# Performance work log

Measured on AMD Instinct MI355X. Metric: run time of the kernel, lower is better.

Reference implementation:

```python
import jax, jax.numpy as jnp
import numpy as np

N_NODES = 100000
N_EDGES = 1600000
IN_FEATS, HIDDEN, OUT_MU, OUT_LV = 256, 128, 64, 64


def setup_inputs() -> dict:
    key = jax.random.key(0)
    ks = jax.random.split(key, 8)
    X = jax.random.normal(ks[0], (N_NODES, IN_FEATS), dtype=jnp.float32)
    edge_index = jax.random.randint(ks[1], (2, N_EDGES), 0, N_NODES, dtype=jnp.int64)
    def glorot(k, shape):
        lim = np.sqrt(6.0 / (shape[0] + shape[1])).astype(np.float32)
        return jax.random.uniform(k, shape, jnp.float32, -lim, lim)
    W1 = glorot(ks[2], (IN_FEATS, HIDDEN))
    b1 = jnp.zeros((HIDDEN,), jnp.float32)
    Wmu = glorot(ks[3], (HIDDEN, OUT_MU))
    bmu = jnp.zeros((OUT_MU,), jnp.float32)
    Wlv = glorot(ks[4], (HIDDEN, OUT_LV))
    blv = jnp.zeros((OUT_LV,), jnp.float32)
    return {"X": X, "edge_index": edge_index, "W1": W1, "b1": b1,
            "Wmu": Wmu, "bmu": bmu, "Wlv": Wlv, "blv": blv}


def _gcn_norm(edge_index, num_nodes):
    # Add self-loops (PyG GCNConv default) and compute symmetric normalization.
    loop = jnp.arange(num_nodes, dtype=edge_index.dtype)
    row = jnp.concatenate([edge_index[0], loop])  # source
    col = jnp.concatenate([edge_index[1], loop])  # target
    deg = jax.ops.segment_sum(jnp.ones_like(col, dtype=jnp.float32), col,
                              num_segments=num_nodes)
    dinv = jnp.where(deg > 0, jax.lax.rsqrt(deg), 0.0)
    norm = dinv[row] * dinv[col]  # [E+N]
    return row, col, norm


def _gcn_conv(x, W, b, row, col, norm, num_nodes):
    # Linear transform, then normalized sparse neighbor aggregation at targets.
    h = x @ W                                   # [N, F_out]
    msg = h[row] * norm[:, None]                # gather + scale, [E+N, F_out]
    out = jax.ops.segment_sum(msg, col, num_segments=num_nodes)
    return out + b


def reference(X, edge_index, W1, b1, Wmu, bmu, Wlv, blv):
    n = X.shape[0]
    row, col, norm = _gcn_norm(edge_index, n)
    H = jax.nn.relu(_gcn_conv(X, W1, b1, row, col, norm, n))
    mu = _gcn_conv(H, Wmu, bmu, row, col, norm, n)
    lv = _gcn_conv(H, Wlv, blv, row, col, norm, n)
    return (mu, lv)
```

## Files before the change

kernel.cpp:

```cpp
#include <hip/hip_runtime.h>
#include <hip/hip_bf16.h>
#include <cstdint>

#define N_FEATS_IN 256
#define HID 128
#define OUTF 64
#define SITEMS 8

typedef __bf16 bf16x8 __attribute__((ext_vector_type(8)));
typedef __bf16 bf16x2 __attribute__((ext_vector_type(2)));
typedef float f32x4 __attribute__((ext_vector_type(4)));


__global__ __launch_bounds__(256) void count_deg_kernel(const int* __restrict__ ei, int E,
    int* __restrict__ deg, int* __restrict__ erank) {
  int e = blockIdx.x * 256 + threadIdx.x;
  if (e < E) erank[e] = atomicAdd(&deg[ei[E + e]], 1);
}

__global__ __launch_bounds__(256) void dinv_kernel(const int* __restrict__ deg,
                                                   float* __restrict__ dinv, int n) {
  int i = blockIdx.x * 256 + threadIdx.x;
  if (i < n) dinv[i] = rsqrtf((float)(deg[i] + 1));
}


__global__ __launch_bounds__(256) void scan_part_kernel(const int* __restrict__ cnt, int n,
                                                        int* __restrict__ bsum) {
  __shared__ int ts[256];
  const int t = threadIdx.x;
  int base = (blockIdx.x * 256 + t) * SITEMS;
  int s = 0;
#pragma unroll
  for (int i = 0; i < SITEMS; ++i) {
    int idx = base + i;
    if (idx < n) s += cnt[idx];
  }
  ts[t] = s;
  __syncthreads();
  for (int off = 128; off > 0; off >>= 1) {
    if (t < off) ts[t] += ts[t + off];
    __syncthreads();
  }
  if (t == 0) bsum[blockIdx.x] = ts[0];
}

__global__ __launch_bounds__(256) void scan_bsum_kernel(int* __restrict__ bsum, int nb) {
  __shared__ int ts[256];
  const int t = threadIdx.x;
  int v = (t < nb) ? bsum[t] : 0;
  ts[t] = v;
  __syncthreads();
  for (int off = 1; off < 256; off <<= 1) {
    int u = (t >= off) ? ts[t - off] : 0;
    __syncthreads();
    ts[t] += u;
    __syncthreads();
  }
  if (t < nb) bsum[t] = ts[t] - v;
}

__global__ __launch_bounds__(256) void scan_final_kernel(const int* __restrict__ cnt, int n,
    const int* __restrict__ bsum, int* __restrict__ ptr) {
  __shared__ int ts[256];
  const int t = threadIdx.x;
  int base = (blockIdx.x * 256 + t) * SITEMS;
  int loc[SITEMS];
  int s = 0;
#pragma unroll
  for (int i = 0; i < SITEMS; ++i) {
    int idx = base + i;
    loc[i] = (idx < n) ? cnt[idx] : 0;
    s += loc[i];
  }
  ts[t] = s;
  __syncthreads();
  for (int off = 1; off < 256; off <<= 1) {
    int u = (t >= off) ? ts[t - off] : 0;
    __syncthreads();
    ts[t] += u;
    __syncthreads();
  }
  int run = bsum[blockIdx.x] + ts[t] - s;
#pragma unroll
  for (int i = 0; i < SITEMS; ++i) {
    int idx = base + i;
    if (idx < n) ptr[idx] = run;
    run += loc[i];
  }
  if (base < n && base + SITEMS >= n) ptr[n] = run;
}


__global__ __launch_bounds__(256) void fill_kernel(const int* __restrict__ ei, int E,
    const int* __restrict__ ptr, const int* __restrict__ erank,
    const float* __restrict__ dinv, int2* __restrict__ erec) {
  int e = blockIdx.x * 256 + threadIdx.x;
  if (e < E) {
    int r = ei[e];
    int c = ei[E + e];
    int pos = ptr[c] + erank[e];
    int2 rec;
    rec.x = r;
    rec.y = __float_as_int(dinv[r] * dinv[c]);
    erec[pos] = rec;
  }
}


__global__ __launch_bounds__(256) void pack_w1_kernel(const float* __restrict__ W,
                                                      __bf16* __restrict__ Wp) {
  int idx = blockIdx.x * 256 + threadIdx.x;
  if (idx >= 32768) return;
  int j = idx & 7, l = (idx >> 3) & 63, t = (idx >> 9) & 7, s = idx >> 12;
  int k = s * 32 + (l >> 4) * 8 + j;
  int n = t * 16 + (l & 15);
  Wp[idx] = (__bf16)W[k * HID + n];
}

__global__ __launch_bounds__(256) void pack_wc_kernel(const float* __restrict__ Wmu,
    const float* __restrict__ Wlv, __bf16* __restrict__ Wp) {
  int idx = blockIdx.x * 256 + threadIdx.x;
  if (idx >= 16384) return;
  int j = idx & 7, l = (idx >> 3) & 63, t = (idx >> 9) & 7, s = idx >> 12;
  int k = s * 32 + (l >> 4) * 8 + j;
  int g = t * 16 + (l & 15);
  float v = (g < OUTF) ? Wmu[k * OUTF + g] : Wlv[k * OUTF + (g - OUTF)];
  Wp[idx] = (__bf16)v;
}


__global__ __launch_bounds__(256) void gemm1_mfma(const float* __restrict__ X,
    const __bf16* __restrict__ Wp, __bf16* __restrict__ Yb, int nrows) {
  const int lane = threadIdx.x & 63;
  const int wave = threadIdx.x >> 6;
  const int rb = blockIdx.x * 128 + wave * 32;
  const int lm = lane & 15;
  const int q = lane >> 4;

  f32x4 acc[2][8];
#pragma unroll
  for (int m = 0; m < 2; ++m)
#pragma unroll
    for (int t = 0; t < 8; ++t) acc[m][t] = (f32x4)0.f;

  int r0 = min(rb + lm, nrows - 1);
  int r1 = min(rb + 16 + lm, nrows - 1);
  const float* x0 = X + (size_t)r0 * N_FEATS_IN + q * 8;
  const float* x1 = X + (size_t)r1 * N_FEATS_IN + q * 8;
  const bf16x8* wp = (const bf16x8*)Wp;

#pragma unroll
  for (int s = 0; s < 8; ++s) {
    float4 u0 = ((const float4*)(x0 + s * 32))[0];
    float4 v0 = ((const float4*)(x0 + s * 32))[1];
    float4 u1 = ((const float4*)(x1 + s * 32))[0];
    float4 v1 = ((const float4*)(x1 + s * 32))[1];
    bf16x8 a0, a1;
    a0[0] = (__bf16)u0.x; a0[1] = (__bf16)u0.y; a0[2] = (__bf16)u0.z; a0[3] = (__bf16)u0.w;
    a0[4] = (__bf16)v0.x; a0[5] = (__bf16)v0.y; a0[6] = (__bf16)v0.z; a0[7] = (__bf16)v0.w;
    a1[0] = (__bf16)u1.x; a1[1] = (__bf16)u1.y; a1[2] = (__bf16)u1.z; a1[3] = (__bf16)u1.w;
    a1[4] = (__bf16)v1.x; a1[5] = (__bf16)v1.y; a1[6] = (__bf16)v1.z; a1[7] = (__bf16)v1.w;
#pragma unroll
    for (int t = 0; t < 8; ++t) {
      bf16x8 b = wp[(s * 8 + t) * 64 + lane];
      acc[0][t] = __builtin_amdgcn_mfma_f32_16x16x32_bf16(a0, b, acc[0][t], 0, 0, 0);
      acc[1][t] = __builtin_amdgcn_mfma_f32_16x16x32_bf16(a1, b, acc[1][t], 0, 0, 0);
    }
  }
#pragma unroll
  for (int m = 0; m < 2; ++m) {
    int rowbase = rb + m * 16 + q * 4;
#pragma unroll
    for (int t = 0; t < 8; ++t) {
#pragma unroll
      for (int r = 0; r < 4; ++r) {
        int row = rowbase + r;
        if (row < nrows) Yb[(size_t)row * HID + t * 16 + lm] = (__bf16)acc[m][t][r];
      }
    }
  }
}


__global__ __launch_bounds__(64) void agg_kernel(const __bf16* __restrict__ Fin,
    const int* __restrict__ ptr, const int2* __restrict__ erec,
    const float* __restrict__ dinv, const float* __restrict__ bias,
    __bf16* __restrict__ Fout, int do_relu) {
  const int c = blockIdx.x;
  const int t = threadIdx.x;
  const float d = dinv[c];
  bf16x2 sv = ((const bf16x2*)(Fin + (size_t)c * HID))[t];
  float ax = d * d * (float)sv[0];
  float ay = d * d * (float)sv[1];
  const int beg = ptr[c], end = ptr[c + 1];
  int e = beg;
  for (; e + 4 <= end; e += 4) {
    int2 p0 = erec[e], p1 = erec[e + 1], p2 = erec[e + 2], p3 = erec[e + 3];
    float n0 = __int_as_float(p0.y), n1 = __int_as_float(p1.y);
    float n2 = __int_as_float(p2.y), n3 = __int_as_float(p3.y);
    bf16x2 v0 = ((const bf16x2*)(Fin + (size_t)p0.x * HID))[t];
    bf16x2 v1 = ((const bf16x2*)(Fin + (size_t)p1.x * HID))[t];
    bf16x2 v2 = ((const bf16x2*)(Fin + (size_t)p2.x * HID))[t];
    bf16x2 v3 = ((const bf16x2*)(Fin + (size_t)p3.x * HID))[t];
    ax = fmaf(n0, (float)v0[0], ax); ay = fmaf(n0, (float)v0[1], ay);
    ax = fmaf(n1, (float)v1[0], ax); ay = fmaf(n1, (float)v1[1], ay);
    ax = fmaf(n2, (float)v2[0], ax); ay = fmaf(n2, (float)v2[1], ay);
    ax = fmaf(n3, (float)v3[0], ax); ay = fmaf(n3, (float)v3[1], ay);
  }
  for (; e < end; ++e) {
    int2 p = erec[e];
    float nn = __int_as_float(p.y);
    bf16x2 v = ((const bf16x2*)(Fin + (size_t)p.x * HID))[t];
    ax = fmaf(nn, (float)v[0], ax);
    ay = fmaf(nn, (float)v[1], ay);
  }
  if (do_relu) {
    ax = fmaxf(ax + bias[2 * t], 0.f);
    ay = fmaxf(ay + bias[2 * t + 1], 0.f);
  }
  bf16x2 o;
  o[0] = (__bf16)ax;
  o[1] = (__bf16)ay;
  ((bf16x2*)(Fout + (size_t)c * HID))[t] = o;
}


__global__ __launch_bounds__(256) void gemm2_mfma(const __bf16* __restrict__ Gb,
    const __bf16* __restrict__ Wp, const float* __restrict__ bmu,
    const float* __restrict__ blv, float* __restrict__ out, int nrows) {
  const int lane = threadIdx.x & 63;
  const int wave = threadIdx.x >> 6;
  const int rb = blockIdx.x * 128 + wave * 32;
  const int lm = lane & 15;
  const int q = lane >> 4;

  f32x4 acc[2][8];
#pragma unroll
  for (int m = 0; m < 2; ++m)
#pragma unroll
    for (int t = 0; t < 8; ++t) acc[m][t] = (f32x4)0.f;

  int r0 = min(rb + lm, nrows - 1);
  int r1 = min(rb + 16 + lm, nrows - 1);
  const __bf16* g0 = Gb + (size_t)r0 * HID + q * 8;
  const __bf16* g1 = Gb + (size_t)r1 * HID + q * 8;
  const bf16x8* wp = (const bf16x8*)Wp;

#pragma unroll
  for (int s = 0; s < 4; ++s) {
    bf16x8 a0 = *(const bf16x8*)(g0 + s * 32);
    bf16x8 a1 = *(const bf16x8*)(g1 + s * 32);
#pragma unroll
    for (int t = 0; t < 8; ++t) {
      bf16x8 b = wp[(s * 8 + t) * 64 + lane];
      acc[0][t] = __builtin_amdgcn_mfma_f32_16x16x32_bf16(a0, b, acc[0][t], 0, 0, 0);
      acc[1][t] = __builtin_amdgcn_mfma_f32_16x16x32_bf16(a1, b, acc[1][t], 0, 0, 0);
    }
  }
#pragma unroll
  for (int m = 0; m < 2; ++m) {
    int rowbase = rb + m * 16 + q * 4;
#pragma unroll
    for (int t = 0; t < 8; ++t) {
      int g = t * 16 + lm;
      float bv = (g < OUTF) ? bmu[g] : blv[g - OUTF];
      float* ob = (g < OUTF) ? (out + g) : (out + (size_t)nrows * OUTF + (g - OUTF));
#pragma unroll
      for (int r = 0; r < 4; ++r) {
        int row = rowbase + r;
        if (row < nrows) ob[(size_t)row * OUTF] = acc[m][t][r] + bv;
      }
    }
  }
}


extern "C" void kernel_launch(void* const* d_in, const int* in_sizes, int n_in,
                              void* d_out, int out_size, void* d_ws, size_t ws_size,
                              hipStream_t stream) {
  const float* X   = (const float*)d_in[0];
  const int*   ei  = (const int*)d_in[1];
  const float* W1  = (const float*)d_in[2];
  const float* b1  = (const float*)d_in[3];
  const float* Wmu = (const float*)d_in[4];
  const float* bmu = (const float*)d_in[5];
  const float* Wlv = (const float*)d_in[6];
  const float* blv = (const float*)d_in[7];
  float* out = (float*)d_out;

  const int N = in_sizes[0] / N_FEATS_IN;
  const int E = in_sizes[1] / 2;

  char* ws = (char*)d_ws;
  size_t off = 0;
  auto alloc = [&](size_t bytes) -> void* {
    void* p = ws + off;
    off += (bytes + 255) & ~(size_t)255;
    return p;
  };
  __bf16* Yb  = (__bf16*)alloc((size_t)N * HID * 2);
  __bf16* Hb  = (__bf16*)alloc((size_t)N * HID * 2);
  float* dinv = (float*)alloc((size_t)N * 4);
  int*   deg  = (int*)alloc((size_t)N * 4);
  int*   ptr  = (int*)alloc((size_t)(N + 1) * 4);
  int*   erank = (int*)alloc((size_t)E * 4);
  int2*  erec = (int2*)alloc((size_t)E * 8);
  __bf16* W1p = (__bf16*)alloc(32768 * 2);
  __bf16* Wcp = (__bf16*)alloc(16384 * 2);
  int*   bsum = (int*)alloc(256 * 4);
  (void)ws_size; (void)n_in; (void)out_size;

  hipMemsetAsync(deg, 0, (size_t)N * 4, stream);

  int ge = (E + 255) / 256;
  int gn = (N + 255) / 256;
  int nb = (N + 256 * SITEMS - 1) / (256 * SITEMS);
  count_deg_kernel<<<ge, 256, 0, stream>>>(ei, E, deg, erank);
  dinv_kernel<<<gn, 256, 0, stream>>>(deg, dinv, N);
  scan_part_kernel<<<nb, 256, 0, stream>>>(deg, N, bsum);
  scan_bsum_kernel<<<1, 256, 0, stream>>>(bsum, nb);
  scan_final_kernel<<<nb, 256, 0, stream>>>(deg, N, bsum, ptr);
  fill_kernel<<<ge, 256, 0, stream>>>(ei, E, ptr, erank, dinv, erec);
  pack_w1_kernel<<<128, 256, 0, stream>>>(W1, W1p);
  pack_wc_kernel<<<64, 256, 0, stream>>>(Wmu, Wlv, Wcp);

  int gblk = (N + 127) / 128;
  gemm1_mfma<<<gblk, 256, 0, stream>>>(X, W1p, Yb, N);
  agg_kernel<<<N, 64, 0, stream>>>(Yb, ptr, erec, dinv, b1, Hb, 1);
  agg_kernel<<<N, 64, 0, stream>>>(Hb, ptr, erec, dinv, b1, Yb, 0);
  gemm2_mfma<<<gblk, 256, 0, stream>>>(Yb, Wcp, bmu, blv, out, N);
}
```

Measured before the change: 481.3 us.

## Privatize degree counters per XCD to keep edge-count atomics in local L2

Degree counting now uses one counter array per XCD, picked via the hardware XCC_ID register, with relaxed workgroup-scope atomics. Each edge's local rank is tagged with its XCD index. A new combine kernel turns the per-XCD counts into exclusive offsets plus a total degree, and the fill kernel adds that offset when placing edges into CSR order. The goal is to avoid costly cross-XCD device-scope atomics. In exchange it adds a larger memset (eight counter arrays), an extra kernel, and relies on workgroup-scope atomics staying coherent across workgroups on the same XCD.

```diff
diff --git a/kernel.cpp b/kernel.cpp
--- a/kernel.cpp
+++ b/kernel.cpp
@@ -6,16 +6,44 @@
 #define HID 128
 #define OUTF 64
 #define SITEMS 8
+#define NXCD 8
 
 typedef __bf16 bf16x8 __attribute__((ext_vector_type(8)));
 typedef __bf16 bf16x2 __attribute__((ext_vector_type(2)));
 typedef float f32x4 __attribute__((ext_vector_type(4)));
 
+__device__ __forceinline__ int xcc_id() {
+  int x;
+  asm volatile("s_getreg_b32 %0, hwreg(HW_REG_XCC_ID, 0, 32)" : "=s"(x));
+  return x & (NXCD - 1);
+}
+
 
 __global__ __launch_bounds__(256) void count_deg_kernel(const int* __restrict__ ei, int E,
-    int* __restrict__ deg, int* __restrict__ erank) {
+    int N, int* __restrict__ cnt8, int* __restrict__ erank) {
   int e = blockIdx.x * 256 + threadIdx.x;
-  if (e < E) erank[e] = atomicAdd(&deg[ei[E + e]], 1);
+  int x = xcc_id();
+  if (e < E) {
+    int c = ei[E + e];
+    int lr = __hip_atomic_fetch_add(&cnt8[(size_t)x * N + c], 1,
+                                    __ATOMIC_RELAXED, __HIP_MEMORY_SCOPE_WORKGROUP);
+    erank[e] = lr | (x << 28);
+  }
+}
+
+__global__ __launch_bounds__(256) void combine_kernel(int* __restrict__ cnt8,
+                                                      int* __restrict__ deg, int n) {
+  int c = blockIdx.x * 256 + threadIdx.x;
+  if (c < n) {
+    int s = 0;
+#pragma unroll
+    for (int x = 0; x < NXCD; ++x) {
+      int v = cnt8[(size_t)x * n + c];
+      cnt8[(size_t)x * n + c] = s;
+      s += v;
+    }
+    deg[c] = s;
+  }
 }
 
 __global__ __launch_bounds__(256) void dinv_kernel(const int* __restrict__ deg,
@@ -92,14 +120,17 @@
 }
 
 
-__global__ __launch_bounds__(256) void fill_kernel(const int* __restrict__ ei, int E,
-    const int* __restrict__ ptr, const int* __restrict__ erank,
+__global__ __launch_bounds__(256) void fill_kernel(const int* __restrict__ ei, int E, int N,
+    const int* __restrict__ ptr, const int* __restrict__ offs, const int* __restrict__ erank,
     const float* __restrict__ dinv, int2* __restrict__ erec) {
   int e = blockIdx.x * 256 + threadIdx.x;
   if (e < E) {
     int r = ei[e];
     int c = ei[E + e];
-    int pos = ptr[c] + erank[e];
+    int er = erank[e];
+    int x = er >> 28;
+    int lr = er & 0x0FFFFFFF;
+    int pos = ptr[c] + offs[(size_t)x * N + c] + lr;
     int2 rec;
     rec.x = r;
     rec.y = __float_as_int(dinv[r] * dinv[c]);
@@ -304,6 +335,7 @@
   float* dinv = (float*)alloc((size_t)N * 4);
   int*   deg  = (int*)alloc((size_t)N * 4);
   int*   ptr  = (int*)alloc((size_t)(N + 1) * 4);
+  int*   cnt8 = (int*)alloc((size_t)NXCD * N * 4);
   int*   erank = (int*)alloc((size_t)E * 4);
   int2*  erec = (int2*)alloc((size_t)E * 8);
   __bf16* W1p = (__bf16*)alloc(32768 * 2);
@@ -311,17 +343,18 @@
   int*   bsum = (int*)alloc(256 * 4);
   (void)ws_size; (void)n_in; (void)out_size;
 
-  hipMemsetAsync(deg, 0, (size_t)N * 4, stream);
+  hipMemsetAsync(cnt8, 0, (size_t)NXCD * N * 4, stream);
 
   int ge = (E + 255) / 256;
   int gn = (N + 255) / 256;
   int nb = (N + 256 * SITEMS - 1) / (256 * SITEMS);
-  count_deg_kernel<<<ge, 256, 0, stream>>>(ei, E, deg, erank);
+  count_deg_kernel<<<ge, 256, 0, stream>>>(ei, E, N, cnt8, erank);
+  combine_kernel<<<gn, 256, 0, stream>>>(cnt8, deg, N);
   dinv_kernel<<<gn, 256, 0, stream>>>(deg, dinv, N);
   scan_part_kernel<<<nb, 256, 0, stream>>>(deg, N, bsum);
   scan_bsum_kernel<<<1, 256, 0, stream>>>(bsum, nb);
   scan_final_kernel<<<nb, 256, 0, stream>>>(deg, N, bsum, ptr);
-  fill_kernel<<<ge, 256, 0, stream>>>(ei, E, ptr, erank, dinv, erec);
+  fill_kernel<<<ge, 256, 0, stream>>>(ei, E, N, ptr, cnt8, erank, dinv, erec);
   pack_w1_kernel<<<128, 256, 0, stream>>>(W1, W1p);
   pack_wc_kernel<<<64, 256, 0, stream>>>(Wmu, Wlv, Wcp);
 
```

Measured after the change: 482.0 us. Within noise of the previous version (+0.2%).
